# Kernel tuning notes

Hardware: AMD Instinct MI355X
Metric: run time of the kernel (lower is better)

## Reference

```python
import jax, jax.numpy as jnp
import numpy as np

N_NODES = 12288
N_FEATURES = 256
KEY_DIM = 128
N_GRAPHS = 192


def setup_inputs() -> dict:
    key = jax.random.key(0)
    k1, k2, k3, k4, k5 = jax.random.split(key, 5)
    node_out = jax.random.normal(k1, (N_NODES, N_FEATURES), dtype=jnp.float32)
    batch = jnp.sort(jax.random.randint(k2, (N_NODES,), 0, N_GRAPHS, dtype=jnp.int64))
    # xavier_uniform: limit = sqrt(6 / (fan_in + fan_out))
    lim_qk = float(np.sqrt(6.0 / (N_FEATURES + KEY_DIM)))
    lim_v = float(np.sqrt(6.0 / (N_FEATURES + N_FEATURES)))
    query_weight = jax.random.uniform(k3, (N_FEATURES, KEY_DIM), jnp.float32, -lim_qk, lim_qk)
    key_weight = jax.random.uniform(k4, (N_FEATURES, KEY_DIM), jnp.float32, -lim_qk, lim_qk)
    value_weight = jax.random.uniform(k5, (N_FEATURES, N_FEATURES), jnp.float32, -lim_v, lim_v)
    return {
        "node_out": node_out,
        "batch": batch,
        "query_weight": query_weight,
        "key_weight": key_weight,
        "value_weight": value_weight,
    }


def reference(node_out, batch, query_weight, key_weight, value_weight):
    n_features = node_out.shape[1]
    Q = node_out @ query_weight            # [N, K]
    K = node_out @ key_weight              # [N, K]
    V = node_out @ value_weight            # [N, F]
    # NOTE: original scales by sqrt(n_features), not sqrt(key_dim)
    scores = (Q @ K.T) / jnp.sqrt(jnp.asarray(n_features, dtype=Q.dtype))  # [N, N]
    mask = batch[:, None] == batch[None, :]  # block-diagonal per-graph mask
    scores = jnp.where(mask, scores, -jnp.inf)
    attn = jax.nn.softmax(scores, axis=-1)   # every row has >=1 valid entry
    context = attn @ V                        # [N, F]
    return jax.ops.segment_sum(context, batch, num_segments=N_GRAPHS)  # [G, F]
```

## Files before the change

kernel.cpp:

```cpp
#include <hip/hip_runtime.h>
#include <hip/hip_bf16.h>

#define N_NODES  12288
#define N_FEAT   256
#define KDIM     128
#define N_GRAPHS 192
#define NMAX     112
#define KSTRIDE_U 68
#define XS_STRIDE_U 132

#define WS_STARTS 0
#define WS_WBUF   1024
#define WS_QB     (WS_WBUF + N_NODES * 4)
#define WS_KB     (WS_QB + N_NODES * 64 * 4)
#define WS_WT     (WS_KB + N_NODES * 64 * 4)

typedef __bf16 bf16x8 __attribute__((ext_vector_type(8)));
typedef float  f32x4  __attribute__((ext_vector_type(4)));

__device__ __forceinline__ unsigned bf16_rne(float f) {
  unsigned u = __float_as_uint(f);
  return (u + 0x7FFFu + ((u >> 16) & 1u)) >> 16;
}
__device__ __forceinline__ unsigned pack_bf16(float lo, float hi) {
  return bf16_rne(lo) | (bf16_rne(hi) << 16);
}
__device__ __forceinline__ float bf_lo(unsigned u) { return __uint_as_float(u << 16); }
__device__ __forceinline__ float bf_hi(unsigned u) { return __uint_as_float(u & 0xFFFF0000u); }

__global__ __launch_bounds__(64) void wt_prep_k(const float* __restrict__ Wq,
                                                const float* __restrict__ Wk,
                                                const int* __restrict__ batch,
                                                unsigned* __restrict__ Wt,
                                                int* __restrict__ starts) {
  const int n = blockIdx.x;
  const int t = threadIdx.x;
  const float* src = (n < KDIM) ? (Wq + n) : (Wk + (n - KDIM));
  float f0 = src[(4 * t + 0) * KDIM];
  float f1 = src[(4 * t + 1) * KDIM];
  float f2 = src[(4 * t + 2) * KDIM];
  float f3 = src[(4 * t + 3) * KDIM];
  Wt[n * 128 + 2 * t]     = pack_bf16(f0, f1);
  Wt[n * 128 + 2 * t + 1] = pack_bf16(f2, f3);

  if (t == 0 && n <= N_GRAPHS) {
    int lo = 0, hi = N_NODES;
    while (lo < hi) {
      int mid = (lo + hi) >> 1;
      if (batch[mid] < n) lo = mid + 1; else hi = mid;
    }
    starts[n] = lo;
  }
}

__global__ __launch_bounds__(256) void qk_proj_k(const float* __restrict__ X,
                                                 const unsigned* __restrict__ Wt,
                                                 unsigned* __restrict__ Qb,
                                                 unsigned* __restrict__ Kb) {
  __shared__ unsigned Xs_u[16 * XS_STRIDE_U];

  const int tid  = threadIdx.x;
  const int lane = tid & 63;
  const int wv   = tid >> 6;
  const int r0   = blockIdx.x * 16;
  const int l15  = lane & 15;
  const int quad = lane >> 4;

  {
    const int row = tid >> 4, seg = tid & 15;
    const float* xp = &X[(size_t)(r0 + row) * N_FEAT + seg * 16];
    float4 a = *(const float4*)xp;
    float4 b = *(const float4*)(xp + 4);
    float4 c = *(const float4*)(xp + 8);
    float4 d = *(const float4*)(xp + 12);
    unsigned* dst = &Xs_u[row * XS_STRIDE_U + seg * 8];
    *(uint4*)dst       = make_uint4(pack_bf16(a.x, a.y), pack_bf16(a.z, a.w),
                                    pack_bf16(b.x, b.y), pack_bf16(b.z, b.w));
    *(uint4*)(dst + 4) = make_uint4(pack_bf16(c.x, c.y), pack_bf16(c.z, c.w),
                                    pack_bf16(d.x, d.y), pack_bf16(d.z, d.w));
  }
  __syncthreads();

  f32x4 acc[4];
#pragma unroll
  for (int ni = 0; ni < 4; ni++) acc[ni] = (f32x4){0.f, 0.f, 0.f, 0.f};

#pragma unroll
  for (int ks = 0; ks < 8; ks++) {
    bf16x8 a = *(const bf16x8*)&Xs_u[l15 * XS_STRIDE_U + ks * 16 + quad * 4];
    bf16x8 b[4];
#pragma unroll
    for (int ni = 0; ni < 4; ni++)
      b[ni] = *(const bf16x8*)&Wt[(size_t)(wv * 64 + ni * 16 + l15) * 128 + ks * 16 + quad * 4];
#pragma unroll
    for (int ni = 0; ni < 4; ni++)
      acc[ni] = __builtin_amdgcn_mfma_f32_16x16x32_bf16(a, b[ni], acc[ni], 0, 0, 0);
  }

  unsigned* dst = (wv < 2) ? Qb : Kb;
  const float scale = (wv < 2) ? 0.0625f : 1.0f;
  const int colbase = (wv & 1) * 64;
#pragma unroll
  for (int ni = 0; ni < 4; ni++) {
    const int col = colbase + ni * 16 + l15;
#pragma unroll
    for (int e = 0; e < 4; e++) {
      const int row = r0 + quad * 4 + e;
      unsigned b = bf16_rne(acc[ni][e] * scale);
      unsigned partner = __shfl_xor((int)b, 1);
      if ((lane & 1) == 0)
        dst[row * 64 + (col >> 1)] = b | (partner << 16);
    }
  }
}

__global__ __launch_bounds__(512) void attn_pool_k(const float* __restrict__ X,
                                                   const int* __restrict__ starts,
                                                   const unsigned* __restrict__ Qb,
                                                   const unsigned* __restrict__ Kb,
                                                   const float* __restrict__ Wv,
                                                   float* __restrict__ out,
                                                   float* __restrict__ wbuf) {
  __shared__ unsigned Ks_u[NMAX * KSTRIDE_U];
  __shared__ float    w_lds[8][NMAX];
  __shared__ float    red[2][256];
  __shared__ float    Us[256];

  const int tid  = threadIdx.x;
  const int lane = tid & 63;
  const int wv   = tid >> 6;
  const int l15  = lane & 15;
  const int quad = lane >> 4;
  const int g    = blockIdx.x;

  const int i0 = starts[g];
  const int n  = starts[g + 1] - i0;
  const float BIG = 1e30f;
  const bool fast = (n <= NMAX);

  if (fast) {
    for (int idx = tid; idx < n * 16; idx += 512) {
      int j = idx >> 4, c = idx & 15;
      *(uint4*)&Ks_u[j * KSTRIDE_U + 4 * c] = *(const uint4*)&Kb[(size_t)(i0 + j) * 64 + 4 * c];
    }
    __syncthreads();

    float wl[7];
#pragma unroll
    for (int f = 0; f < 7; f++) wl[f] = 0.f;

    const int ns = (n + 15) >> 4;
    if (wv < ns) {
      const int s = wv;
      const int arow = min(s * 16 + l15, n - 1);
      const unsigned* qrow = &Qb[(size_t)(i0 + arow) * 64];
      bf16x8 au[4];
#pragma unroll
      for (int ks = 0; ks < 4; ks++)
        au[ks] = *(const bf16x8*)&qrow[ks * 16 + quad * 4];

      f32x4 acc[7];
#pragma unroll
      for (int f = 0; f < 7; f++) acc[f] = (f32x4){0.f, 0.f, 0.f, 0.f};
#pragma unroll
      for (int f = 0; f < 7; f++) {
#pragma unroll
        for (int ks = 0; ks < 4; ks++) {
          bf16x8 bu = *(const bf16x8*)&Ks_u[(f * 16 + l15) * KSTRIDE_U + ks * 16 + quad * 4];
          acc[f] = __builtin_amdgcn_mfma_f32_16x16x32_bf16(au[ks], bu, acc[f], 0, 0, 0);
        }
      }
#pragma unroll
      for (int f = 0; f < 7; f++)
        if (f * 16 + l15 >= n) {
          acc[f][0] = -BIG; acc[f][1] = -BIG; acc[f][2] = -BIG; acc[f][3] = -BIG;
        }

#pragma unroll
      for (int e = 0; e < 4; e++) {
        float m = -BIG;
#pragma unroll
        for (int f = 0; f < 7; f++) m = fmaxf(m, acc[f][e]);
        m = fmaxf(m, __shfl_xor(m, 1));
        m = fmaxf(m, __shfl_xor(m, 2));
        m = fmaxf(m, __shfl_xor(m, 4));
        m = fmaxf(m, __shfl_xor(m, 8));
        float p[7], l = 0.f;
#pragma unroll
        for (int f = 0; f < 7; f++) { p[f] = __expf(acc[f][e] - m); l += p[f]; }
        l += __shfl_xor(l, 1);
        l += __shfl_xor(l, 2);
        l += __shfl_xor(l, 4);
        l += __shfl_xor(l, 8);
        const int row = s * 16 + quad * 4 + e;
        float inv = (row < n) ? (1.f / l) : 0.f;
#pragma unroll
        for (int f = 0; f < 7; f++) wl[f] = fmaf(p[f], inv, wl[f]);
      }
    }

#pragma unroll
    for (int f = 0; f < 7; f++) {
      wl[f] += __shfl_xor(wl[f], 16);
      wl[f] += __shfl_xor(wl[f], 32);
    }
    if (lane < 16) {
#pragma unroll
      for (int f = 0; f < 7; f++) w_lds[wv][f * 16 + lane] = wl[f];
    }
    __syncthreads();

    if (tid < NMAX) {
      float t = 0.f;
#pragma unroll
      for (int k = 0; k < 8; k++) t += w_lds[k][tid];
      w_lds[0][tid] = t;
    }
    __syncthreads();
  } else {
    for (int idx = tid; idx < n; idx += 512) wbuf[i0 + idx] = 0.f;
    __syncthreads();
    for (int lr = wv; lr < n; lr += 8) {
      const uint4* qp4 = (const uint4*)&Qb[(size_t)(i0 + lr) * 64];
      float m_run = -BIG, l_run = 0.f;
      for (int jb = 0; jb < n; jb += 64) {
        int j = jb + lane;
        int jc = min(j, n - 1);
        const uint4* kp4 = (const uint4*)&Kb[(size_t)(i0 + jc) * 64];
        float s = 0.f;
        for (int c = 0; c < 16; c++) {
          uint4 Q1 = qp4[c];
          uint4 K1 = kp4[c];
          s = fmaf(bf_lo(Q1.x), bf_lo(K1.x), s); s = fmaf(bf_hi(Q1.x), bf_hi(K1.x), s);
          s = fmaf(bf_lo(Q1.y), bf_lo(K1.y), s); s = fmaf(bf_hi(Q1.y), bf_hi(K1.y), s);
          s = fmaf(bf_lo(Q1.z), bf_lo(K1.z), s); s = fmaf(bf_hi(Q1.z), bf_hi(K1.z), s);
          s = fmaf(bf_lo(Q1.w), bf_lo(K1.w), s); s = fmaf(bf_hi(Q1.w), bf_hi(K1.w), s);
        }
        if (j >= n) s = -BIG;
        float mc = s;
        for (int off = 32; off; off >>= 1) mc = fmaxf(mc, __shfl_xor(mc, off));
        float m_new = fmaxf(m_run, mc);
        float lc = __expf(s - m_new);
        for (int off = 32; off; off >>= 1) lc += __shfl_xor(lc, off);
        l_run = l_run * __expf(m_run - m_new) + lc;
        m_run = m_new;
      }
      float inv = 1.f / l_run;
      for (int jb = 0; jb < n; jb += 64) {
        int j = jb + lane;
        int jc = min(j, n - 1);
        const uint4* kp4 = (const uint4*)&Kb[(size_t)(i0 + jc) * 64];
        float s = 0.f;
        for (int c = 0; c < 16; c++) {
          uint4 Q1 = qp4[c];
          uint4 K1 = kp4[c];
          s = fmaf(bf_lo(Q1.x), bf_lo(K1.x), s); s = fmaf(bf_hi(Q1.x), bf_hi(K1.x), s);
          s = fmaf(bf_lo(Q1.y), bf_lo(K1.y), s); s = fmaf(bf_hi(Q1.y), bf_hi(K1.y), s);
          s = fmaf(bf_lo(Q1.z), bf_lo(K1.z), s); s = fmaf(bf_hi(Q1.z), bf_hi(K1.z), s);
          s = fmaf(bf_lo(Q1.w), bf_lo(K1.w), s); s = fmaf(bf_hi(Q1.w), bf_hi(K1.w), s);
        }
        if (j < n) atomicAdd(&wbuf[i0 + j], __expf(s - m_run) * inv);
      }
    }
    __threadfence();
    __syncthreads();
  }

  const int f  = tid & 255;
  const int jp = tid >> 8;
  float ua = 0.f, ub = 0.f;
  if (fast) {
    int j = jp;
    for (; j + 2 < n; j += 4) {
      ua = fmaf(w_lds[0][j],     X[(size_t)(i0 + j) * N_FEAT + f], ua);
      ub = fmaf(w_lds[0][j + 2], X[(size_t)(i0 + j + 2) * N_FEAT + f], ub);
    }
    for (; j < n; j += 2)
      ua = fmaf(w_lds[0][j], X[(size_t)(i0 + j) * N_FEAT + f], ua);
  } else {
    for (int j = jp; j < n; j += 2) {
      float wj = atomicAdd(&wbuf[i0 + j], 0.f);
      ua = fmaf(wj, X[(size_t)(i0 + j) * N_FEAT + f], ua);
    }
  }
  red[jp][f] = ua + ub;
  __syncthreads();
  if (jp == 0) Us[f] = red[0][f] + red[1][f];
  __syncthreads();

  const int k0 = jp * 128;
  const float* wp = Wv + (size_t)k0 * N_FEAT + f;
  const float* us = &Us[k0];
  float a0 = 0.f, a1 = 0.f, a2 = 0.f, a3 = 0.f;
#pragma unroll 8
  for (int k = 0; k < 128; k += 4) {
    a0 = fmaf(us[k],     wp[(size_t)k * N_FEAT], a0);
    a1 = fmaf(us[k + 1], wp[(size_t)(k + 1) * N_FEAT], a1);
    a2 = fmaf(us[k + 2], wp[(size_t)(k + 2) * N_FEAT], a2);
    a3 = fmaf(us[k + 3], wp[(size_t)(k + 3) * N_FEAT], a3);
  }
  __syncthreads();
  red[jp][f] = (a0 + a1) + (a2 + a3);
  __syncthreads();
  if (jp == 0) out[g * N_FEAT + f] = red[0][f] + red[1][f];
}

extern "C" void kernel_launch(void* const* d_in, const int* in_sizes, int n_in,
                              void* d_out, int out_size, void* d_ws, size_t ws_size,
                              hipStream_t stream) {
  const float* X     = (const float*)d_in[0];
  const int*   batch = (const int*)d_in[1];
  const float* Wq    = (const float*)d_in[2];
  const float* Wk    = (const float*)d_in[3];
  const float* Wv    = (const float*)d_in[4];
  float* out = (float*)d_out;

  char* ws = (char*)d_ws;
  int*      starts = (int*)(ws + WS_STARTS);
  float*    wbuf   = (float*)(ws + WS_WBUF);
  unsigned* Qb     = (unsigned*)(ws + WS_QB);
  unsigned* Kb     = (unsigned*)(ws + WS_KB);
  unsigned* Wt     = (unsigned*)(ws + WS_WT);

  wt_prep_k<<<256, 64, 0, stream>>>(Wq, Wk, batch, Wt, starts);
  qk_proj_k<<<N_NODES / 16, 256, 0, stream>>>(X, Wt, Qb, Kb);
  attn_pool_k<<<N_GRAPHS, 512, 0, stream>>>(X, starts, Qb, Kb, Wv, out, wbuf);
}
```

Baseline: 98.27 us.

## Fuse QK projection into per-graph attention kernel, keep Q/K in LDS

Removes the separate qk_proj_k launch. Each per-graph block now converts its own X rows to bf16 in LDS, computes Q and K with MFMA, and keeps them in shared memory instead of writing them to global memory and reading them back. Graphs larger than NMAX still go through a chunked projection that writes to global Q/K. The pooling loop also gets four accumulators instead of two. The cost is much higher LDS use per block, which limits occupancy, and only 192 blocks share the projection work, so parallelism is lower than the 768-block projection kernel it replaces.

```diff
diff --git a/kernel.cpp b/kernel.cpp
--- a/kernel.cpp
+++ b/kernel.cpp
@@ -53,74 +53,16 @@
   }
 }
 
-__global__ __launch_bounds__(256) void qk_proj_k(const float* __restrict__ X,
-                                                 const unsigned* __restrict__ Wt,
-                                                 unsigned* __restrict__ Qb,
-                                                 unsigned* __restrict__ Kb) {
-  __shared__ unsigned Xs_u[16 * XS_STRIDE_U];
-
-  const int tid  = threadIdx.x;
-  const int lane = tid & 63;
-  const int wv   = tid >> 6;
-  const int r0   = blockIdx.x * 16;
-  const int l15  = lane & 15;
-  const int quad = lane >> 4;
-
-  {
-    const int row = tid >> 4, seg = tid & 15;
-    const float* xp = &X[(size_t)(r0 + row) * N_FEAT + seg * 16];
-    float4 a = *(const float4*)xp;
-    float4 b = *(const float4*)(xp + 4);
-    float4 c = *(const float4*)(xp + 8);
-    float4 d = *(const float4*)(xp + 12);
-    unsigned* dst = &Xs_u[row * XS_STRIDE_U + seg * 8];
-    *(uint4*)dst       = make_uint4(pack_bf16(a.x, a.y), pack_bf16(a.z, a.w),
-                                    pack_bf16(b.x, b.y), pack_bf16(b.z, b.w));
-    *(uint4*)(dst + 4) = make_uint4(pack_bf16(c.x, c.y), pack_bf16(c.z, c.w),
-                                    pack_bf16(d.x, d.y), pack_bf16(d.z, d.w));
-  }
-  __syncthreads();
-
-  f32x4 acc[4];
-#pragma unroll
-  for (int ni = 0; ni < 4; ni++) acc[ni] = (f32x4){0.f, 0.f, 0.f, 0.f};
-
-#pragma unroll
-  for (int ks = 0; ks < 8; ks++) {
-    bf16x8 a = *(const bf16x8*)&Xs_u[l15 * XS_STRIDE_U + ks * 16 + quad * 4];
-    bf16x8 b[4];
-#pragma unroll
-    for (int ni = 0; ni < 4; ni++)
-      b[ni] = *(const bf16x8*)&Wt[(size_t)(wv * 64 + ni * 16 + l15) * 128 + ks * 16 + quad * 4];
-#pragma unroll
-    for (int ni = 0; ni < 4; ni++)
-      acc[ni] = __builtin_amdgcn_mfma_f32_16x16x32_bf16(a, b[ni], acc[ni], 0, 0, 0);
-  }
-
-  unsigned* dst = (wv < 2) ? Qb : Kb;
-  const float scale = (wv < 2) ? 0.0625f : 1.0f;
-  const int colbase = (wv & 1) * 64;
-#pragma unroll
-  for (int ni = 0; ni < 4; ni++) {
-    const int col = colbase + ni * 16 + l15;
-#pragma unroll
-    for (int e = 0; e < 4; e++) {
-      const int row = r0 + quad * 4 + e;
-      unsigned b = bf16_rne(acc[ni][e] * scale);
-      unsigned partner = __shfl_xor((int)b, 1);
-      if ((lane & 1) == 0)
-        dst[row * 64 + (col >> 1)] = b | (partner << 16);
-    }
-  }
-}
-
-__global__ __launch_bounds__(512) void attn_pool_k(const float* __restrict__ X,
-                                                   const int* __restrict__ starts,
-                                                   const unsigned* __restrict__ Qb,
-                                                   const unsigned* __restrict__ Kb,
-                                                   const float* __restrict__ Wv,
-                                                   float* __restrict__ out,
-                                                   float* __restrict__ wbuf) {
+__global__ __launch_bounds__(512) void attn_fused_k(const float* __restrict__ X,
+                                                    const int* __restrict__ starts,
+                                                    const unsigned* __restrict__ Wt,
+                                                    const float* __restrict__ Wv,
+                                                    float* __restrict__ out,
+                                                    unsigned* __restrict__ Qb,
+                                                    unsigned* __restrict__ Kb,
+                                                    float* __restrict__ wbuf) {
+  __shared__ unsigned Xs_u[NMAX * XS_STRIDE_U];
+  __shared__ unsigned Qs_u[NMAX * KSTRIDE_U];
   __shared__ unsigned Ks_u[NMAX * KSTRIDE_U];
   __shared__ float    w_lds[8][NMAX];
   __shared__ float    red[2][256];
@@ -138,10 +80,66 @@
   const float BIG = 1e30f;
   const bool fast = (n <= NMAX);
 
+  bf16x8 bq0[8], bq1[8];
+  {
+    const unsigned* w0 = &Wt[(size_t)((2 * wv + 0) * 16 + l15) * 128 + quad * 4];
+    const unsigned* w1 = &Wt[(size_t)((2 * wv + 1) * 16 + l15) * 128 + quad * 4];
+#pragma unroll
+    for (int ks = 0; ks < 8; ks++) {
+      bq0[ks] = *(const bf16x8*)&w0[ks * 16];
+      bq1[ks] = *(const bf16x8*)&w1[ks * 16];
+    }
+  }
+  unsigned* dst_lds   = (wv < 4) ? Qs_u : Ks_u;
+  const float scale   = (wv < 4) ? 0.0625f : 1.0f;
+  const int cb0 = ((2 * wv + 0) & 7) * 16;
+  const int cb1 = ((2 * wv + 1) & 7) * 16;
+
   if (fast) {
-    for (int idx = tid; idx < n * 16; idx += 512) {
-      int j = idx >> 4, c = idx & 15;
-      *(uint4*)&Ks_u[j * KSTRIDE_U + 4 * c] = *(const uint4*)&Kb[(size_t)(i0 + j) * 64 + 4 * c];
+    const int ns   = (n + 15) >> 4;
+    const int npad = ns * 16;
+
+    for (int idx = tid; idx < npad * 16; idx += 512) {
+      int row = idx >> 4, seg = idx & 15;
+      unsigned* dst = &Xs_u[row * XS_STRIDE_U + seg * 8];
+      if (row < n) {
+        const float* xp = &X[(size_t)(i0 + row) * N_FEAT + seg * 16];
+        float4 a = *(const float4*)xp;
+        float4 b = *(const float4*)(xp + 4);
+        float4 c = *(const float4*)(xp + 8);
+        float4 d = *(const float4*)(xp + 12);
+        *(uint4*)dst       = make_uint4(pack_bf16(a.x, a.y), pack_bf16(a.z, a.w),
+                                        pack_bf16(b.x, b.y), pack_bf16(b.z, b.w));
+        *(uint4*)(dst + 4) = make_uint4(pack_bf16(c.x, c.y), pack_bf16(c.z, c.w),
+                                        pack_bf16(d.x, d.y), pack_bf16(d.z, d.w));
+      } else {
+        *(uint4*)dst       = make_uint4(0u, 0u, 0u, 0u);
+        *(uint4*)(dst + 4) = make_uint4(0u, 0u, 0u, 0u);
+      }
+    }
+    __syncthreads();
+
+    for (int s = 0; s < ns; s++) {
+      f32x4 acc0 = (f32x4){0.f, 0.f, 0.f, 0.f};
+      f32x4 acc1 = (f32x4){0.f, 0.f, 0.f, 0.f};
+#pragma unroll
+      for (int ks = 0; ks < 8; ks++) {
+        bf16x8 a = *(const bf16x8*)&Xs_u[(s * 16 + l15) * XS_STRIDE_U + ks * 16 + quad * 4];
+        acc0 = __builtin_amdgcn_mfma_f32_16x16x32_bf16(a, bq0[ks], acc0, 0, 0, 0);
+        acc1 = __builtin_amdgcn_mfma_f32_16x16x32_bf16(a, bq1[ks], acc1, 0, 0, 0);
+      }
+#pragma unroll
+      for (int e = 0; e < 4; e++) {
+        const int row = s * 16 + quad * 4 + e;
+        unsigned b0 = bf16_rne(acc0[e] * scale);
+        unsigned p0 = __shfl_xor((int)b0, 1);
+        unsigned b1 = bf16_rne(acc1[e] * scale);
+        unsigned p1 = __shfl_xor((int)b1, 1);
+        if ((lane & 1) == 0) {
+          dst_lds[row * KSTRIDE_U + ((cb0 + l15) >> 1)] = b0 | (p0 << 16);
+          dst_lds[row * KSTRIDE_U + ((cb1 + l15) >> 1)] = b1 | (p1 << 16);
+        }
+      }
     }
     __syncthreads();
 
@@ -149,15 +147,13 @@
 #pragma unroll
     for (int f = 0; f < 7; f++) wl[f] = 0.f;
 
-    const int ns = (n + 15) >> 4;
     if (wv < ns) {
       const int s = wv;
       const int arow = min(s * 16 + l15, n - 1);
-      const unsigned* qrow = &Qb[(size_t)(i0 + arow) * 64];
       bf16x8 au[4];
 #pragma unroll
       for (int ks = 0; ks < 4; ks++)
-        au[ks] = *(const bf16x8*)&qrow[ks * 16 + quad * 4];
+        au[ks] = *(const bf16x8*)&Qs_u[arow * KSTRIDE_U + ks * 16 + quad * 4];
 
       f32x4 acc[7];
 #pragma unroll
@@ -219,7 +215,57 @@
     __syncthreads();
   } else {
     for (int idx = tid; idx < n; idx += 512) wbuf[i0 + idx] = 0.f;
-    __syncthreads();
+
+    for (int c0 = 0; c0 < n; c0 += NMAX) {
+      const int cn  = min(NMAX, n - c0);
+      const int cns = (cn + 15) >> 4;
+      __syncthreads();
+      for (int idx = tid; idx < cns * 16 * 16; idx += 512) {
+        int row = idx >> 4, seg = idx & 15;
+        unsigned* dst = &Xs_u[row * XS_STRIDE_U + seg * 8];
+        if (row < cn) {
+          const float* xp = &X[(size_t)(i0 + c0 + row) * N_FEAT + seg * 16];
+          float4 a = *(const float4*)xp;
+          float4 b = *(const float4*)(xp + 4);
+          float4 c = *(const float4*)(xp + 8);
+          float4 d = *(const float4*)(xp + 12);
+          *(uint4*)dst       = make_uint4(pack_bf16(a.x, a.y), pack_bf16(a.z, a.w),
+                                          pack_bf16(b.x, b.y), pack_bf16(b.z, b.w));
+          *(uint4*)(dst + 4) = make_uint4(pack_bf16(c.x, c.y), pack_bf16(c.z, c.w),
+                                          pack_bf16(d.x, d.y), pack_bf16(d.z, d.w));
+        } else {
+          *(uint4*)dst       = make_uint4(0u, 0u, 0u, 0u);
+          *(uint4*)(dst + 4) = make_uint4(0u, 0u, 0u, 0u);
+        }
+      }
+      __syncthreads();
+      unsigned* dstg = (wv < 4) ? Qb : Kb;
+      for (int s = 0; s < cns; s++) {
+        f32x4 acc0 = (f32x4){0.f, 0.f, 0.f, 0.f};
+        f32x4 acc1 = (f32x4){0.f, 0.f, 0.f, 0.f};
+#pragma unroll
+        for (int ks = 0; ks < 8; ks++) {
+          bf16x8 a = *(const bf16x8*)&Xs_u[(s * 16 + l15) * XS_STRIDE_U + ks * 16 + quad * 4];
+          acc0 = __builtin_amdgcn_mfma_f32_16x16x32_bf16(a, bq0[ks], acc0, 0, 0, 0);
+          acc1 = __builtin_amdgcn_mfma_f32_16x16x32_bf16(a, bq1[ks], acc1, 0, 0, 0);
+        }
+#pragma unroll
+        for (int e = 0; e < 4; e++) {
+          const int row = s * 16 + quad * 4 + e;
+          unsigned b0 = bf16_rne(acc0[e] * scale);
+          unsigned p0 = __shfl_xor((int)b0, 1);
+          unsigned b1 = bf16_rne(acc1[e] * scale);
+          unsigned p1 = __shfl_xor((int)b1, 1);
+          if ((lane & 1) == 0 && row < cn) {
+            dstg[(size_t)(i0 + c0 + row) * 64 + ((cb0 + l15) >> 1)] = b0 | (p0 << 16);
+            dstg[(size_t)(i0 + c0 + row) * 64 + ((cb1 + l15) >> 1)] = b1 | (p1 << 16);
+          }
+        }
+      }
+    }
+    __threadfence();
+    __syncthreads();
+
     for (int lr = wv; lr < n; lr += 8) {
       const uint4* qp4 = (const uint4*)&Qb[(size_t)(i0 + lr) * 64];
       float m_run = -BIG, l_run = 0.f;
@@ -268,22 +314,24 @@
 
   const int f  = tid & 255;
   const int jp = tid >> 8;
-  float ua = 0.f, ub = 0.f;
+  float u0 = 0.f, u1 = 0.f, u2 = 0.f, u3 = 0.f;
   if (fast) {
     int j = jp;
-    for (; j + 2 < n; j += 4) {
-      ua = fmaf(w_lds[0][j],     X[(size_t)(i0 + j) * N_FEAT + f], ua);
-      ub = fmaf(w_lds[0][j + 2], X[(size_t)(i0 + j + 2) * N_FEAT + f], ub);
+    for (; j + 6 < n; j += 8) {
+      u0 = fmaf(w_lds[0][j],     X[(size_t)(i0 + j) * N_FEAT + f], u0);
+      u1 = fmaf(w_lds[0][j + 2], X[(size_t)(i0 + j + 2) * N_FEAT + f], u1);
+      u2 = fmaf(w_lds[0][j + 4], X[(size_t)(i0 + j + 4) * N_FEAT + f], u2);
+      u3 = fmaf(w_lds[0][j + 6], X[(size_t)(i0 + j + 6) * N_FEAT + f], u3);
     }
     for (; j < n; j += 2)
-      ua = fmaf(w_lds[0][j], X[(size_t)(i0 + j) * N_FEAT + f], ua);
+      u0 = fmaf(w_lds[0][j], X[(size_t)(i0 + j) * N_FEAT + f], u0);
   } else {
     for (int j = jp; j < n; j += 2) {
       float wj = atomicAdd(&wbuf[i0 + j], 0.f);
-      ua = fmaf(wj, X[(size_t)(i0 + j) * N_FEAT + f], ua);
-    }
-  }
-  red[jp][f] = ua + ub;
+      u0 = fmaf(wj, X[(size_t)(i0 + j) * N_FEAT + f], u0);
+    }
+  }
+  red[jp][f] = (u0 + u1) + (u2 + u3);
   __syncthreads();
   if (jp == 0) Us[f] = red[0][f] + red[1][f];
   __syncthreads();
@@ -323,6 +371,5 @@
   unsigned* Wt     = (unsigned*)(ws + WS_WT);
 
   wt_prep_k<<<256, 64, 0, stream>>>(Wq, Wk, batch, Wt, starts);
-  qk_proj_k<<<N_NODES / 16, 256, 0, stream>>>(X, Wt, Qb, Kb);
-  attn_pool_k<<<N_GRAPHS, 512, 0, stream>>>(X, starts, Qb, Kb, Wv, out, wbuf);
-}
+  attn_fused_k<<<N_GRAPHS, 512, 0, stream>>>(X, starts, Wt, Wv, out, Qb, Kb, wbuf);
+}
```

Result: faster. 86.67 us (-11.8%).
